# Kernel tuning notes

Measured on AMD Instinct MI355X. Metric: run time of the kernel, lower is better.

Reference implementation:

```python
import jax, jax.numpy as jnp
import numpy as np

B, C, Lc, Vc = 16, 8, 30, 10000
Lp, Vp = 64, 2000
N_IV = 128
BETA_C = 0.7
BETA_P = 0.7


def setup_inputs() -> dict:
    key = jax.random.key(0)
    ks = jax.random.split(key, 9)
    pred_captions = jax.random.normal(ks[0], (B, C, Lc, Vc), jnp.float32)
    gt_captions = jax.random.randint(ks[1], (B, C, Lc), 0, Vc)
    gt_cap_lens = jax.random.randint(ks[2], (B, C), 1, Lc + 1).astype(jnp.int32)
    gt_caps_count = jax.random.randint(ks[3], (B,), 1, C + 1).astype(jnp.int32)
    pred_program = jax.random.normal(ks[4], (B, Lp, Vp), jnp.float32)
    gt_program = jax.random.randint(ks[5], (B, Lp), 0, Vp)
    gt_prog_len = jax.random.randint(ks[6], (B,), 1, Lp + 1).astype(jnp.int32)
    # intervals [N,2,1]: sort along dim 1 so end >= start (well-conditioned union)
    pred_intervals = jnp.sort(jax.random.uniform(ks[7], (N_IV, 2, 1), jnp.float32), axis=1)
    gt_intervals = jnp.sort(jax.random.uniform(ks[8], (N_IV, 2, 1), jnp.float32), axis=1)
    scores = jnp.ones((3,), jnp.float32)  # config.combination_scores
    return dict(gt_captions=gt_captions, gt_cap_lens=gt_cap_lens,
                pred_captions=pred_captions, gt_program=gt_program,
                gt_prog_len=gt_prog_len, pred_program=pred_program,
                gt_intervals=gt_intervals, pred_intervals=pred_intervals,
                gt_caps_count=gt_caps_count, scores=scores)


def _sentlen_loss(logits, targets, lens, item_mask, beta):
    """SentenceLengthLoss ('mean'): -sum_t logsoftmax[t, tgt_t] / len_i**beta, / n_items.
    logits [..., T, V]; targets [..., T] int; lens [...] int; item_mask [...] bool.
    Masked form is exactly equivalent to the torch ragged gather/concat packing.
    """
    T = logits.shape[-2]
    tok_mask = (jnp.arange(T) < lens[..., None]) & item_mask[..., None]  # [..., T]
    logp = jax.nn.log_softmax(logits, axis=-1)
    tok_lp = jnp.take_along_axis(logp, targets[..., None], axis=-1)[..., 0]  # [..., T]
    w = jnp.where(item_mask,
                  1.0 / jnp.maximum(lens, 1).astype(jnp.float32) ** beta,
                  0.0)  # per-sentence weight 1/len**beta
    loss_sum = -jnp.sum(w[..., None] * jnp.where(tok_mask, tok_lp, 0.0))
    n_items = jnp.sum(item_mask.astype(jnp.float32))
    return loss_sum / n_items


def _iou_loss(pred_iv, gt_iv):
    # pred_iv, gt_iv: [N, 2, 1] (start, end)
    p0, p1 = pred_iv[:, 0, 0], pred_iv[:, 1, 0]
    g0, g1 = gt_iv[:, 0, 0], gt_iv[:, 1, 0]
    inter = jnp.clip(jnp.minimum(p1, g1) - jnp.maximum(p0, g0), 0.0)
    union = jnp.maximum(p1, g1) - jnp.minimum(p0, g0)
    return 1.0 - jnp.sum(inter / union) / pred_iv.shape[0]


def reference(gt_captions, gt_cap_lens, pred_captions, gt_program, gt_prog_len,
              pred_program, gt_intervals, pred_intervals, gt_caps_count, scores):
    # captions: caption i of video j is active iff i < gt_caps_count[j]
    cap_item_mask = jnp.arange(pred_captions.shape[1])[None, :] < gt_caps_count[:, None]
    cap_loss = _sentlen_loss(pred_captions, gt_captions, gt_cap_lens,
                             cap_item_mask, BETA_C)
    # program: one sequence per batch element, all active
    prog_item_mask = jnp.ones((pred_program.shape[0],), bool)
    prog_loss = _sentlen_loss(pred_program, gt_program, gt_prog_len,
                              prog_item_mask, BETA_P)
    iou_loss = _iou_loss(pred_intervals, gt_intervals)
    losses = jnp.stack([cap_loss, prog_loss, iou_loss])
    loss = jnp.sum(scores * losses)
    return (loss, cap_loss, prog_loss, iou_loss)
```

## Files before the change

### kernel.cpp

```cpp
#include <hip/hip_runtime.h>
#include <math.h>

#define B   16
#define C   8
#define LC  30
#define VC  10000
#define LP  64
#define VP  2000
#define N_IV 128
#define BETA 0.7f

constexpr int CAP_ROWS    = B * C * LC;
constexpr int PROG_ROWS   = B * LP;
constexpr int PROG_BLOCKS = PROG_ROWS / 4;
constexpr int N4C = VC / 4;
constexpr int KC  = (N4C + 255) / 256;
constexpr int N4P = VP / 4;
constexpr int KP  = (N4P + 63) / 64;

__global__ __launch_bounds__(256) void rows_kernel(
    const float* __restrict__ pred_cap,  const int* __restrict__ gt_cap,
    const int*  __restrict__ cap_lens,   const int* __restrict__ caps_count,
    const float* __restrict__ pred_prog, const int* __restrict__ gt_prog,
    const int*  __restrict__ prog_len,
    float* __restrict__ cap_part, float* __restrict__ prog_part)
{
    __shared__ float ssum[4];

    const int bid = blockIdx.x;
    const int tid = threadIdx.x;

    if (bid < CAP_ROWS) {
        const int b   = bid / (C * LC);
        const int rem = bid % (C * LC);
        const int c   = rem / LC;
        const int t   = rem % LC;
        const int len = cap_lens[b * C + c];
        if (c >= caps_count[b] || t >= len) {
            if (tid == 0) cap_part[bid] = 0.0f;
            return;
        }
        const float* row = pred_cap + (size_t)bid * VC;
        const int   tgt     = gt_cap[bid];
        const float logit_t = row[tgt];

        const float4* row4 = (const float4*)row;
        float4 v[KC];
        #pragma unroll
        for (int k = 0; k < KC; k++) {
            const int j = tid + k * 256;
            if (j < N4C) v[k] = row4[j];
            else v[k] = make_float4(-INFINITY, -INFINITY, -INFINITY, -INFINITY);
        }

        float s = 0.0f;
        #pragma unroll
        for (int k = 0; k < KC; k++)
            s += __expf(v[k].x) + __expf(v[k].y)
               + __expf(v[k].z) + __expf(v[k].w);
        #pragma unroll
        for (int off = 32; off; off >>= 1) s += __shfl_xor(s, off, 64);

        const int wid = tid >> 6;
        if ((tid & 63) == 0) ssum[wid] = s;
        __syncthreads();

        if (tid == 0) {
            const float S   = ssum[0] + ssum[1] + ssum[2] + ssum[3];
            const float lse = __logf(S);
            const float w   = __expf(-BETA * __logf((float)len));
            cap_part[bid] = -w * (logit_t - lse);
        }
    } else {
        const int pb   = bid - CAP_ROWS;
        const int lane = tid & 63;
        const int wid  = tid >> 6;
        const int r    = pb * 4 + wid;
        const int b    = r / LP;
        const int t    = r % LP;
        const int len  = prog_len[b];
        if (t >= len) {
            if (lane == 0) prog_part[r] = 0.0f;
            return;
        }
        const float* row = pred_prog + (size_t)r * VP;
        const int   tgt     = gt_prog[r];
        const float logit_t = row[tgt];

        const float4* row4 = (const float4*)row;
        float4 v[KP];
        #pragma unroll
        for (int k = 0; k < KP; k++) {
            const int j = lane + k * 64;
            if (j < N4P) v[k] = row4[j];
            else v[k] = make_float4(-INFINITY, -INFINITY, -INFINITY, -INFINITY);
        }

        float s = 0.0f;
        #pragma unroll
        for (int k = 0; k < KP; k++)
            s += __expf(v[k].x) + __expf(v[k].y)
               + __expf(v[k].z) + __expf(v[k].w);
        #pragma unroll
        for (int off = 32; off; off >>= 1) s += __shfl_xor(s, off, 64);

        if (lane == 0) {
            const float lse = __logf(s);
            const float w   = __expf(-BETA * __logf((float)len));
            prog_part[r] = -w * (logit_t - lse);
        }
    }
}

__device__ inline float wave_sum(float v) {
    #pragma unroll
    for (int off = 32; off; off >>= 1) v += __shfl_xor(v, off, 64);
    return v;
}

__global__ __launch_bounds__(256) void finish_kernel(
    const float* __restrict__ cap_part, const float* __restrict__ prog_part,
    const int*  __restrict__ caps_count,
    const float* __restrict__ pred_iv, const float* __restrict__ gt_iv,
    const float* __restrict__ scores, float* __restrict__ out)
{
    const int tid = threadIdx.x;

    const float4* cp4 = (const float4*)cap_part;
    float cs = 0.0f;
    #pragma unroll
    for (int k = 0; k < 4; k++) {
        const int j = tid + k * 256;
        if (j < CAP_ROWS / 4) {
            const float4 v = cp4[j];
            cs += (v.x + v.y) + (v.z + v.w);
        }
    }
    const float4* pp4 = (const float4*)prog_part;
    const float4 pv = pp4[tid];
    float ps = (pv.x + pv.y) + (pv.z + pv.w);

    float is = 0.0f;
    if (tid < N_IV) {
        const float p0 = pred_iv[tid * 2 + 0];
        const float p1 = pred_iv[tid * 2 + 1];
        const float g0 = gt_iv[tid * 2 + 0];
        const float g1 = gt_iv[tid * 2 + 1];
        const float inter = fmaxf(fminf(p1, g1) - fmaxf(p0, g0), 0.0f);
        const float uni   = fmaxf(p1, g1) - fminf(p0, g0);
        is = inter / uni;
    }

    float nc = 0.0f;
    if (tid < B) nc = (float)caps_count[tid];

    cs = wave_sum(cs);
    ps = wave_sum(ps);
    is = wave_sum(is);
    nc = wave_sum(nc);

    __shared__ float red[4][4];
    const int wid = tid >> 6;
    if ((tid & 63) == 0) {
        red[0][wid] = cs; red[1][wid] = ps; red[2][wid] = is; red[3][wid] = nc;
    }
    __syncthreads();

    if (tid == 0) {
        const float CS = red[0][0] + red[0][1] + red[0][2] + red[0][3];
        const float PS = red[1][0] + red[1][1] + red[1][2] + red[1][3];
        const float IS = red[2][0] + red[2][1] + red[2][2] + red[2][3];
        const float NC = red[3][0] + red[3][1] + red[3][2] + red[3][3];

        const float cap_loss  = CS / NC;
        const float prog_loss = PS / (float)B;
        const float iou_loss  = 1.0f - IS / (float)N_IV;
        const float loss = scores[0] * cap_loss + scores[1] * prog_loss
                         + scores[2] * iou_loss;
        out[0] = loss;
        out[1] = cap_loss;
        out[2] = prog_loss;
        out[3] = iou_loss;
    }
}

extern "C" void kernel_launch(void* const* d_in, const int* in_sizes, int n_in,
                              void* d_out, int out_size, void* d_ws, size_t ws_size,
                              hipStream_t stream) {
    const int*   gt_captions    = (const int*)  d_in[0];
    const int*   gt_cap_lens    = (const int*)  d_in[1];
    const float* pred_captions  = (const float*)d_in[2];
    const int*   gt_program     = (const int*)  d_in[3];
    const int*   gt_prog_len    = (const int*)  d_in[4];
    const float* pred_program   = (const float*)d_in[5];
    const float* gt_intervals   = (const float*)d_in[6];
    const float* pred_intervals = (const float*)d_in[7];
    const int*   gt_caps_count  = (const int*)  d_in[8];
    const float* scores         = (const float*)d_in[9];
    float* out = (float*)d_out;

    float* cap_part  = (float*)d_ws;
    float* prog_part = cap_part + CAP_ROWS;

    rows_kernel<<<CAP_ROWS + PROG_BLOCKS, 256, 0, stream>>>(
        pred_captions, gt_captions, gt_cap_lens, gt_caps_count,
        pred_program, gt_program, gt_prog_len,
        cap_part, prog_part);

    finish_kernel<<<1, 256, 0, stream>>>(
        cap_part, prog_part, gt_caps_count,
        pred_intervals, gt_intervals, scores, out);
}
```

Measured before the change: 19.64 us.

## Split each caption row across two blocks and combine partial sums in finish

```diff
diff --git a/kernel.cpp b/kernel.cpp
--- a/kernel.cpp
+++ b/kernel.cpp
@@ -11,10 +11,11 @@
 #define BETA 0.7f
 
 constexpr int CAP_ROWS    = B * C * LC;
+constexpr int CAP_BLOCKS  = CAP_ROWS * 2;
 constexpr int PROG_ROWS   = B * LP;
 constexpr int PROG_BLOCKS = PROG_ROWS / 4;
-constexpr int N4C = VC / 4;
-constexpr int KC  = (N4C + 255) / 256;
+constexpr int N4H = (VC / 2) / 4;
+constexpr int KH  = (N4H + 255) / 256;
 constexpr int N4P = VP / 4;
 constexpr int KP  = (N4P + 63) / 64;
 
@@ -23,39 +24,47 @@
     const int*  __restrict__ cap_lens,   const int* __restrict__ caps_count,
     const float* __restrict__ pred_prog, const int* __restrict__ gt_prog,
     const int*  __restrict__ prog_len,
-    float* __restrict__ cap_part, float* __restrict__ prog_part)
+    float* __restrict__ wv, float* __restrict__ wl,
+    float* __restrict__ s_part, float* __restrict__ prog_part)
 {
     __shared__ float ssum[4];
 
     const int bid = blockIdx.x;
     const int tid = threadIdx.x;
 
-    if (bid < CAP_ROWS) {
-        const int b   = bid / (C * LC);
-        const int rem = bid % (C * LC);
-        const int c   = rem / LC;
-        const int t   = rem % LC;
-        const int len = cap_lens[b * C + c];
-        if (c >= caps_count[b] || t >= len) {
-            if (tid == 0) cap_part[bid] = 0.0f;
+    if (bid < CAP_BLOCKS) {
+        const int row  = bid >> 1;
+        const int half = bid & 1;
+        const int b    = row / (C * LC);
+        const int rem  = row % (C * LC);
+        const int c    = rem / LC;
+        const int t    = rem % LC;
+        const int len  = cap_lens[b * C + c];
+        const bool active = (c < caps_count[b]) && (t < len);
+        if (!active) {
+            if (half == 0 && tid == 0) { wv[row] = 0.0f; wl[row] = 0.0f; }
             return;
         }
-        const float* row = pred_cap + (size_t)bid * VC;
-        const int   tgt     = gt_cap[bid];
-        const float logit_t = row[tgt];
-
-        const float4* row4 = (const float4*)row;
-        float4 v[KC];
-        #pragma unroll
-        for (int k = 0; k < KC; k++) {
+
+        const float* rowp = pred_cap + (size_t)row * VC;
+        float logit_t = 0.0f, w = 0.0f;
+        if (half == 0) {
+            logit_t = rowp[gt_cap[row]];
+            w       = __expf(-BETA * __logf((float)len));
+        }
+
+        const float4* row4 = (const float4*)rowp + half * N4H;
+        float4 v[KH];
+        #pragma unroll
+        for (int k = 0; k < KH; k++) {
             const int j = tid + k * 256;
-            if (j < N4C) v[k] = row4[j];
+            if (j < N4H) v[k] = row4[j];
             else v[k] = make_float4(-INFINITY, -INFINITY, -INFINITY, -INFINITY);
         }
 
         float s = 0.0f;
         #pragma unroll
-        for (int k = 0; k < KC; k++)
+        for (int k = 0; k < KH; k++)
             s += __expf(v[k].x) + __expf(v[k].y)
                + __expf(v[k].z) + __expf(v[k].w);
         #pragma unroll
@@ -66,13 +75,11 @@
         __syncthreads();
 
         if (tid == 0) {
-            const float S   = ssum[0] + ssum[1] + ssum[2] + ssum[3];
-            const float lse = __logf(S);
-            const float w   = __expf(-BETA * __logf((float)len));
-            cap_part[bid] = -w * (logit_t - lse);
+            s_part[bid] = (ssum[0] + ssum[1]) + (ssum[2] + ssum[3]);
+            if (half == 0) { wv[row] = w; wl[row] = w * logit_t; }
         }
     } else {
-        const int pb   = bid - CAP_ROWS;
+        const int pb   = bid - CAP_BLOCKS;
         const int lane = tid & 63;
         const int wid  = tid >> 6;
         const int r    = pb * 4 + wid;
@@ -119,23 +126,26 @@
 }
 
 __global__ __launch_bounds__(256) void finish_kernel(
-    const float* __restrict__ cap_part, const float* __restrict__ prog_part,
+    const float* __restrict__ wv, const float* __restrict__ wl,
+    const float* __restrict__ s_part, const float* __restrict__ prog_part,
     const int*  __restrict__ caps_count,
     const float* __restrict__ pred_iv, const float* __restrict__ gt_iv,
     const float* __restrict__ scores, float* __restrict__ out)
 {
     const int tid = threadIdx.x;
-
-    const float4* cp4 = (const float4*)cap_part;
+    const float2* s2 = (const float2*)s_part;
+
     float cs = 0.0f;
     #pragma unroll
-    for (int k = 0; k < 4; k++) {
-        const int j = tid + k * 256;
-        if (j < CAP_ROWS / 4) {
-            const float4 v = cp4[j];
-            cs += (v.x + v.y) + (v.z + v.w);
-        }
-    }
+    for (int it = 0; it < CAP_ROWS / 256; ++it) {
+        const int r = tid + it * 256;
+        const float w = wv[r];
+        if (w != 0.0f) {
+            const float2 sp = s2[r];
+            cs += w * __logf(sp.x + sp.y) - wl[r];
+        }
+    }
+
     const float4* pp4 = (const float4*)prog_part;
     const float4 pv = pp4[tid];
     float ps = (pv.x + pv.y) + (pv.z + pv.w);
@@ -199,15 +209,17 @@
     const float* scores         = (const float*)d_in[9];
     float* out = (float*)d_out;
 
-    float* cap_part  = (float*)d_ws;
-    float* prog_part = cap_part + CAP_ROWS;
-
-    rows_kernel<<<CAP_ROWS + PROG_BLOCKS, 256, 0, stream>>>(
+    float* wv        = (float*)d_ws;
+    float* wl        = wv + CAP_ROWS;
+    float* s_part    = wl + CAP_ROWS;
+    float* prog_part = s_part + CAP_BLOCKS;
+
+    rows_kernel<<<CAP_BLOCKS + PROG_BLOCKS, 256, 0, stream>>>(
         pred_captions, gt_captions, gt_cap_lens, gt_caps_count,
         pred_program, gt_program, gt_prog_len,
-        cap_part, prog_part);
+        wv, wl, s_part, prog_part);
 
     finish_kernel<<<1, 256, 0, stream>>>(
-        cap_part, prog_part, gt_caps_count,
+        wv, wl, s_part, prog_part, gt_caps_count,
         pred_intervals, gt_intervals, scores, out);
 }
```

New measurement: 26.42 us. +34.5%, slower.
